# Kernel tuning notes

Measured on AMD Instinct MI355X. Metric: run time of the kernel, lower is better.

The kernel has to match this reference:

```python
import jax, jax.numpy as jnp
import numpy as np

# Performer/FAVOR+ style linear attention constants (from module __init__)
A_CONST = 0.1
S_CONST = 1.0
B_CONST = (S_CONST * (1.0 - 4.0 * A_CONST)) ** 0.5  # sqrt(0.6)
C_CONST = -(S_CONST + 1.0) / 2.0                    # -1.0

R = 256     # number of random features
D = 64      # head / feature dim
L = 65536   # sequence length
DV = 64     # value dim
SCALE = 0.125  # keep ||q||^2 ~ 1 so exp stays well-conditioned


def setup_inputs() -> dict:
    key = jax.random.key(0)
    kq, kk, kv, kw = jax.random.split(key, 4)
    Q = jax.random.normal(kq, (D, L), dtype=jnp.float32) * SCALE
    K = jax.random.normal(kk, (D, L), dtype=jnp.float32) * SCALE
    V = jax.random.normal(kv, (L, DV), dtype=jnp.float32)
    W = jax.random.normal(kw, (R, D), dtype=jnp.float32)  # random feature projections
    return {"Q": Q, "K": K, "V": V, "W": W}


def _phi(W, X, c):
    # X: [d, L]; W: [r, d] -> features [r, L]
    d = X.shape[0]
    D_norm = (1.0 - 4.0 * A_CONST) ** (d / 4.0)  # pow(pow(1-4A,0.25), d)
    sq = jnp.sum(X * X, axis=0)                  # [L], diag of X^T X
    return D_norm * jnp.exp(A_CONST + B_CONST * (W @ X) + c * sq)


def reference(Q, K, V, W):
    phiK = _phi(W, K, C_CONST * S_CONST)  # f2: [r, Lk]
    kv = phiK @ V                          # [r, dv]
    phiQ = _phi(W, Q, C_CONST)             # f1: [r, Lq]
    return phiQ.T @ kv                     # [Lq, dv]
```

## Files before the change

kernel.cpp:

```cpp
#include <hip/hip_runtime.h>

typedef _Float16 f16;
typedef __attribute__((ext_vector_type(8))) _Float16 f16x8;
typedef __attribute__((ext_vector_type(4))) _Float16 f16x4;
typedef __attribute__((ext_vector_type(4))) float f32x4;

#define BARRIER()                                              \
    do {                                                       \
        asm volatile("s_waitcnt lgkmcnt(0)" ::: "memory");     \
        __builtin_amdgcn_s_barrier();                          \
        __builtin_amdgcn_sched_barrier(0);                     \
    } while (0)

namespace {
constexpr int kL   = 65536;
constexpr int kR   = 256;
constexpr int kD   = 64;
constexpr int kDV  = 64;

constexpr int kABlocks = 512;
constexpr int kBBlocks = 512;
constexpr int kRBlocks = 128;

constexpr float kAc  = 0.1f;
constexpr float kBc  = 0.7745966692414834f;
constexpr float kDnS = 0.2888816545234944f;
constexpr float kOutScale = 9.5367431640625e-7f;
}

__global__ __launch_bounds__(512, 2)
void favor_kv(const float* __restrict__ Kg, const float* __restrict__ Vg,
              const float* __restrict__ Wg, f16* __restrict__ partials)
{
    __shared__ f16 sXt[64 * 64];
    __shared__ f16 sVt[64 * 64];
    __shared__ f16 sPhi[256 * 64];
    __shared__ float sRed[8 * 64];
    __shared__ float sRedT[64];

    const int tid  = threadIdx.x;
    const int w    = tid >> 6;
    const int lane = tid & 63;
    const int l15  = lane & 15;
    const int lhi  = lane >> 4;
    const int blk  = blockIdx.x;
    const int lblk = blk * 128;

    const int scol  = lane;
    const int dbase = w * 8;

    float ka[2][8], va[2][8];
#pragma unroll
    for (int c = 0; c < 2; ++c) {
        const int l0 = lblk + c * 64;
#pragma unroll
        for (int j = 0; j < 8; ++j) ka[c][j] = Kg[(dbase + j) * kL + l0 + scol];
#pragma unroll
        for (int j = 0; j < 8; ++j) va[c][j] = Vg[(size_t)(l0 + dbase + j) * kDV + scol];
    }

    f16x8 wfrag[2][2];
#pragma unroll
    for (int ri = 0; ri < 2; ++ri)
#pragma unroll
        for (int ks = 0; ks < 2; ++ks) {
            const float* p = Wg + (32 * w + 16 * ri + l15) * kD + 32 * ks + 8 * lhi;
            f16x8 v;
#pragma unroll
            for (int j = 0; j < 8; ++j) v[j] = (f16)p[j];
            wfrag[ri][ks] = v;
        }

    f32x4 acc[4][2];
#pragma unroll
    for (int a = 0; a < 4; ++a)
#pragma unroll
        for (int d = 0; d < 2; ++d) { f32x4 z0 = {0.f, 0.f, 0.f, 0.f}; acc[a][d] = z0; }

    const int wr = w >> 1;
    const int wc = w & 1;

#pragma unroll
    for (int c = 0; c < 2; ++c) {
        {
            float s = 0.f;
            f16x8 hk, hv;
#pragma unroll
            for (int j = 0; j < 8; ++j) {
                const float x = ka[c][j];
                s += x * x;
                hk[j] = (f16)x;
                hv[j] = (f16)va[c][j];
            }
            sRed[w * 64 + scol] = s;
            *(f16x8*)&sXt[scol * 64 + (dbase ^ ((scol & 7) << 3))] = hk;
            *(f16x8*)&sVt[scol * 64 + (dbase ^ ((scol & 7) << 3))] = hv;
        }
        BARRIER();

        {
            float sqv = 0.f;
#pragma unroll
            for (int g = 0; g < 8; ++g) sqv += sRed[g * 64 + lane];
            sRedT[lane] = sqv;
        }

#pragma unroll
        for (int ri = 0; ri < 2; ++ri) {
            f32x4 z[4];
#pragma unroll
            for (int lf = 0; lf < 4; ++lf) { f32x4 z0 = {0.f, 0.f, 0.f, 0.f}; z[lf] = z0; }
            __builtin_amdgcn_s_setprio(1);
#pragma unroll
            for (int ks = 0; ks < 2; ++ks) {
                f16x8 bfr[4];
#pragma unroll
                for (int lf = 0; lf < 4; ++lf) {
                    const int row = 16 * lf + l15;
                    bfr[lf] = *(const f16x8*)&sXt[row * 64 + ((32 * ks + 8 * lhi) ^ ((row & 7) << 3))];
                }
#pragma unroll
                for (int lf = 0; lf < 4; ++lf)
                    z[lf] = __builtin_amdgcn_mfma_f32_16x16x32_f16(bfr[lf], wfrag[ri][ks], z[lf], 0, 0, 0);
            }
            __builtin_amdgcn_s_setprio(0);
            const int r = 32 * w + 16 * ri + l15;
#pragma unroll
            for (int lf = 0; lf < 4; ++lf) {
                const f32x4 sq4 = *(const f32x4*)&sRedT[16 * lf + 4 * lhi];
                f16x4 ph;
#pragma unroll
                for (int j = 0; j < 4; ++j)
                    ph[j] = (f16)(kDnS * __expf(kAc + kBc * z[lf][j] - sq4[j]));
                const int lbase = 16 * lf + 4 * lhi;
                *(f16x4*)&sPhi[r * 64 + (lbase ^ ((r & 7) << 3))] = ph;
            }
        }
        BARRIER();

        __builtin_amdgcn_s_setprio(1);
#pragma unroll
        for (int ks = 0; ks < 2; ++ks) {
            f16x8 af[4], bf[2];
#pragma unroll
            for (int ai = 0; ai < 4; ++ai) {
                const int r = 64 * wr + 16 * ai + l15;
                af[ai] = *(const f16x8*)&sPhi[r * 64 + ((32 * ks + 8 * lhi) ^ ((r & 7) << 3))];
            }
#pragma unroll
            for (int di = 0; di < 2; ++di) {
                const int dv = 32 * wc + 16 * di + l15;
                bf[di] = *(const f16x8*)&sVt[dv * 64 + ((32 * ks + 8 * lhi) ^ ((dv & 7) << 3))];
            }
#pragma unroll
            for (int ai = 0; ai < 4; ++ai)
#pragma unroll
                for (int di = 0; di < 2; ++di)
                    acc[ai][di] = __builtin_amdgcn_mfma_f32_16x16x32_f16(af[ai], bf[di], acc[ai][di], 0, 0, 0);
        }
        __builtin_amdgcn_s_setprio(0);
        if (c == 0) BARRIER();
    }

    f16* po = partials + (size_t)blk * (kR * kDV);
#pragma unroll
    for (int ai = 0; ai < 4; ++ai)
#pragma unroll
        for (int di = 0; di < 2; ++di) {
            const int dv = 32 * wc + 16 * di + l15;
            f16x4 pk;
#pragma unroll
            for (int j = 0; j < 4; ++j) pk[j] = (f16)acc[ai][di][j];
            *(f16x4*)&po[dv * kR + 64 * wr + 16 * ai + 4 * lhi] = pk;
        }
}

__global__ __launch_bounds__(512)
void favor_reduce(const f16* __restrict__ partials, f16* __restrict__ kvT)
{
    __shared__ float sAcc[32][128];
    const int tid  = threadIdx.x;
    const int slot = tid & 15;
    const int g    = tid >> 4;
    const size_t obase = (size_t)blockIdx.x * 128 + slot * 8;

    float a[8] = {0.f, 0.f, 0.f, 0.f, 0.f, 0.f, 0.f, 0.f};
#pragma unroll 4
    for (int i = 0; i < 16; ++i) {
        const int s = g * 16 + i;
        const f16x8 v = *(const f16x8*)&partials[(size_t)s * (kR * kDV) + obase];
#pragma unroll
        for (int j = 0; j < 8; ++j) a[j] += (float)v[j];
    }
#pragma unroll
    for (int j = 0; j < 8; ++j) sAcc[g][slot * 8 + j] = a[j];
    __syncthreads();

    if (tid < 128) {
        float tot = 0.f;
#pragma unroll
        for (int gg = 0; gg < 32; ++gg) tot += sAcc[gg][tid];
        kvT[(size_t)blockIdx.x * 128 + tid] = (f16)tot;
    }
}

__global__ __launch_bounds__(512, 2)
void favor_out(const float* __restrict__ Qg, const float* __restrict__ Wg,
               const f16* __restrict__ kvT, float* __restrict__ outg)
{
    __shared__ f16 sXt[64 * 64];
    __shared__ f16 sPhiT[64 * 256];
    __shared__ f16 sKv[64 * 256];
    __shared__ float sRed[8 * 64];

    const int tid  = threadIdx.x;
    const int w    = tid >> 6;
    const int lane = tid & 63;
    const int l15  = lane & 15;
    const int lhi  = lane >> 4;
    const int blk  = blockIdx.x;
    const int lblk = blk * 128;

    const int scol  = lane;
    const int dbase = w * 8;

    float qa[2][8];
#pragma unroll
    for (int c = 0; c < 2; ++c)
#pragma unroll
        for (int j = 0; j < 8; ++j)
            qa[c][j] = Qg[(dbase + j) * kL + lblk + c * 64 + scol];

    const int kdv  = tid >> 3;
    const int kslt = tid & 7;
    f16x8 kvld[4];
#pragma unroll
    for (int m = 0; m < 4; ++m)
        kvld[m] = *(const f16x8*)&kvT[kdv * kR + kslt * 32 + 8 * m];

    f16x8 wfrag[2][2];
#pragma unroll
    for (int ri = 0; ri < 2; ++ri)
#pragma unroll
        for (int ks = 0; ks < 2; ++ks) {
            const float* p = Wg + (32 * w + 16 * ri + l15) * kD + 32 * ks + 8 * lhi;
            f16x8 v;
#pragma unroll
            for (int j = 0; j < 8; ++j) v[j] = (f16)p[j];
            wfrag[ri][ks] = v;
        }

    const int lfo = w >> 1;
    const int dvh = w & 1;

#pragma unroll
    for (int c = 0; c < 2; ++c) {
        {
            float s = 0.f;
            f16x8 hq;
#pragma unroll
            for (int j = 0; j < 8; ++j) {
                const float x = qa[c][j];
                s += x * x;
                hq[j] = (f16)x;
            }
            sRed[w * 64 + scol] = s;
            *(f16x8*)&sXt[scol * 64 + (dbase ^ ((scol & 7) << 3))] = hq;
        }
        if (c == 0) {
#pragma unroll
            for (int m = 0; m < 4; ++m)
                *(f16x8*)&sKv[kdv * kR + ((kslt * 32 + 8 * m) ^ ((kdv & 7) << 3))] = kvld[m];
        }
        BARRIER();

        float sqv = 0.f;
#pragma unroll
        for (int g = 0; g < 8; ++g) sqv += sRed[g * 64 + lane];
        float sqs[4];
#pragma unroll
        for (int lf = 0; lf < 4; ++lf) sqs[lf] = __shfl(sqv, lf * 16 + l15, 64);

#pragma unroll
        for (int ri = 0; ri < 2; ++ri) {
            f32x4 z[4];
#pragma unroll
            for (int lf = 0; lf < 4; ++lf) { f32x4 z0 = {0.f, 0.f, 0.f, 0.f}; z[lf] = z0; }
            __builtin_amdgcn_s_setprio(1);
#pragma unroll
            for (int ks = 0; ks < 2; ++ks) {
                f16x8 bfr[4];
#pragma unroll
                for (int lf = 0; lf < 4; ++lf) {
                    const int row = 16 * lf + l15;
                    bfr[lf] = *(const f16x8*)&sXt[row * 64 + ((32 * ks + 8 * lhi) ^ ((row & 7) << 3))];
                }
#pragma unroll
                for (int lf = 0; lf < 4; ++lf)
                    z[lf] = __builtin_amdgcn_mfma_f32_16x16x32_f16(wfrag[ri][ks], bfr[lf], z[lf], 0, 0, 0);
            }
            __builtin_amdgcn_s_setprio(0);
            const int r0 = 32 * w + 16 * ri + 4 * lhi;
#pragma unroll
            for (int lf = 0; lf < 4; ++lf) {
                const int lc = 16 * lf + l15;
                f16x4 ph;
#pragma unroll
                for (int j = 0; j < 4; ++j)
                    ph[j] = (f16)(kDnS * __expf(kAc + kBc * z[lf][j] - sqs[lf]));
                *(f16x4*)&sPhiT[lc * 256 + (r0 ^ ((lc & 7) << 3))] = ph;
            }
        }
        BARRIER();

        f32x4 o2[2];
        { f32x4 z0 = {0.f, 0.f, 0.f, 0.f}; o2[0] = z0; o2[1] = z0; }
        const int lrow = 16 * lfo + l15;
        __builtin_amdgcn_s_setprio(1);
#pragma unroll
        for (int ks = 0; ks < 8; ++ks) {
            const f16x8 af = *(const f16x8*)&sPhiT[lrow * 256 + ((32 * ks + 8 * lhi) ^ ((lrow & 7) << 3))];
#pragma unroll
            for (int di = 0; di < 2; ++di) {
                const int dv = 32 * dvh + 16 * di + l15;
                const f16x8 bf = *(const f16x8*)&sKv[dv * kR + ((32 * ks + 8 * lhi) ^ ((dv & 7) << 3))];
                o2[di] = __builtin_amdgcn_mfma_f32_16x16x32_f16(af, bf, o2[di], 0, 0, 0);
            }
        }
        __builtin_amdgcn_s_setprio(0);
        const int l0 = lblk + c * 64;
#pragma unroll
        for (int di = 0; di < 2; ++di)
#pragma unroll
            for (int j = 0; j < 4; ++j) {
                const int ll = 16 * lfo + 4 * lhi + j;
                const int dv = 32 * dvh + 16 * di + l15;
                outg[(size_t)(l0 + ll) * kDV + dv] = o2[di][j] * kOutScale;
            }
        if (c == 0) BARRIER();
    }
}

extern "C" void kernel_launch(void* const* d_in, const int* in_sizes, int n_in,
                              void* d_out, int out_size, void* d_ws, size_t ws_size,
                              hipStream_t stream)
{
    const float* Q = (const float*)d_in[0];
    const float* K = (const float*)d_in[1];
    const float* V = (const float*)d_in[2];
    const float* W = (const float*)d_in[3];
    float* out = (float*)d_out;

    f16* partials = (f16*)d_ws;
    f16* kvT = (f16*)((char*)d_ws + (size_t)kABlocks * kR * kDV * sizeof(f16));

    favor_kv<<<kABlocks, 512, 0, stream>>>(K, V, W, partials);
    favor_reduce<<<kRBlocks, 512, 0, stream>>>(partials, kvT);
    favor_out<<<kBBlocks, 512, 0, stream>>>(Q, W, kvT, out);

    (void)in_sizes; (void)n_in; (void)out_size; (void)ws_size;
}
```

Baseline: 41.63 us.

## Double-buffer staging, fold exp constants, keep kv fragments in registers

Both feature kernels now keep two shared-memory copies of the staged X/V tiles and row norms, so the second chunk can be staged while the first chunk's phi is computed. This cuts one barrier per kernel and lets more work overlap. The constants A and the D-norm factor are folded into a single additive base inside exp, which leaves one FMA plus exp per element. favor_out also loads the kv matrix straight into per-wave register fragments instead of staging it through shared memory, trading register pressure for less LDS traffic and smaller LDS footprint.

New measurement: 42.66 us. 2.5% more time.

```diff
diff --git a/kernel.cpp b/kernel.cpp
--- a/kernel.cpp
+++ b/kernel.cpp
@@ -22,9 +22,8 @@
 constexpr int kBBlocks = 512;
 constexpr int kRBlocks = 128;
 
-constexpr float kAc  = 0.1f;
-constexpr float kBc  = 0.7745966692414834f;
-constexpr float kDnS = 0.2888816545234944f;
+constexpr float kBc   = 0.7745966692414834f;
+constexpr float kBase0 = -1.1417405264f;
 constexpr float kOutScale = 9.5367431640625e-7f;
 }
 
@@ -32,11 +31,11 @@
 void favor_kv(const float* __restrict__ Kg, const float* __restrict__ Vg,
               const float* __restrict__ Wg, f16* __restrict__ partials)
 {
-    __shared__ f16 sXt[64 * 64];
-    __shared__ f16 sVt[64 * 64];
+    __shared__ f16 sXt[2][64 * 64];
+    __shared__ f16 sVt[2][64 * 64];
     __shared__ f16 sPhi[256 * 64];
-    __shared__ float sRed[8 * 64];
-    __shared__ float sRedT[64];
+    __shared__ float sRed[2][8 * 64];
+    __shared__ float sRedT[2][64];
 
     const int tid  = threadIdx.x;
     const int w    = tid >> 6;
@@ -80,31 +79,36 @@
     const int wr = w >> 1;
     const int wc = w & 1;
 
-#pragma unroll
-    for (int c = 0; c < 2; ++c) {
-        {
-            float s = 0.f;
-            f16x8 hk, hv;
-#pragma unroll
-            for (int j = 0; j < 8; ++j) {
-                const float x = ka[c][j];
-                s += x * x;
-                hk[j] = (f16)x;
-                hv[j] = (f16)va[c][j];
-            }
-            sRed[w * 64 + scol] = s;
-            *(f16x8*)&sXt[scol * 64 + (dbase ^ ((scol & 7) << 3))] = hk;
-            *(f16x8*)&sVt[scol * 64 + (dbase ^ ((scol & 7) << 3))] = hv;
-        }
-        BARRIER();
-
-        {
-            float sqv = 0.f;
-#pragma unroll
-            for (int g = 0; g < 8; ++g) sqv += sRed[g * 64 + lane];
-            sRedT[lane] = sqv;
-        }
-
+    auto stage = [&](int c) {
+        float s = 0.f;
+        f16x8 hk, hv;
+#pragma unroll
+        for (int j = 0; j < 8; ++j) {
+            const float x = ka[c][j];
+            s += x * x;
+            hk[j] = (f16)x;
+            hv[j] = (f16)va[c][j];
+        }
+        sRed[c][w * 64 + scol] = s;
+        *(f16x8*)&sXt[c][scol * 64 + (dbase ^ ((scol & 7) << 3))] = hk;
+        *(f16x8*)&sVt[c][scol * 64 + (dbase ^ ((scol & 7) << 3))] = hv;
+    };
+
+    auto norms = [&](int c) {
+        float sqv = 0.f;
+#pragma unroll
+        for (int g = 0; g < 8; ++g) sqv += sRed[c][g * 64 + lane];
+        sRedT[c][lane] = sqv;
+    };
+
+    auto zphi = [&](int c) {
+        f32x4 base4[4];
+#pragma unroll
+        for (int lf = 0; lf < 4; ++lf) {
+            const f32x4 sq4 = *(const f32x4*)&sRedT[c][16 * lf + 4 * lhi];
+#pragma unroll
+            for (int j = 0; j < 4; ++j) base4[lf][j] = kBase0 - sq4[j];
+        }
 #pragma unroll
         for (int ri = 0; ri < 2; ++ri) {
             f32x4 z[4];
@@ -117,7 +121,7 @@
 #pragma unroll
                 for (int lf = 0; lf < 4; ++lf) {
                     const int row = 16 * lf + l15;
-                    bfr[lf] = *(const f16x8*)&sXt[row * 64 + ((32 * ks + 8 * lhi) ^ ((row & 7) << 3))];
+                    bfr[lf] = *(const f16x8*)&sXt[c][row * 64 + ((32 * ks + 8 * lhi) ^ ((row & 7) << 3))];
                 }
 #pragma unroll
                 for (int lf = 0; lf < 4; ++lf)
@@ -127,17 +131,17 @@
             const int r = 32 * w + 16 * ri + l15;
 #pragma unroll
             for (int lf = 0; lf < 4; ++lf) {
-                const f32x4 sq4 = *(const f32x4*)&sRedT[16 * lf + 4 * lhi];
                 f16x4 ph;
 #pragma unroll
                 for (int j = 0; j < 4; ++j)
-                    ph[j] = (f16)(kDnS * __expf(kAc + kBc * z[lf][j] - sq4[j]));
+                    ph[j] = (f16)__expf(fmaf(z[lf][j], kBc, base4[lf][j]));
                 const int lbase = 16 * lf + 4 * lhi;
                 *(f16x4*)&sPhi[r * 64 + (lbase ^ ((r & 7) << 3))] = ph;
             }
         }
-        BARRIER();
-
+    };
+
+    auto pv = [&](int c) {
         __builtin_amdgcn_s_setprio(1);
 #pragma unroll
         for (int ks = 0; ks < 2; ++ks) {
@@ -150,7 +154,7 @@
 #pragma unroll
             for (int di = 0; di < 2; ++di) {
                 const int dv = 32 * wc + 16 * di + l15;
-                bf[di] = *(const f16x8*)&sVt[dv * 64 + ((32 * ks + 8 * lhi) ^ ((dv & 7) << 3))];
+                bf[di] = *(const f16x8*)&sVt[c][dv * 64 + ((32 * ks + 8 * lhi) ^ ((dv & 7) << 3))];
             }
 #pragma unroll
             for (int ai = 0; ai < 4; ++ai)
@@ -159,8 +163,20 @@
                     acc[ai][di] = __builtin_amdgcn_mfma_f32_16x16x32_f16(af[ai], bf[di], acc[ai][di], 0, 0, 0);
         }
         __builtin_amdgcn_s_setprio(0);
-        if (c == 0) BARRIER();
-    }
+    };
+
+    stage(0);
+    BARRIER();
+    norms(0);
+    zphi(0);
+    stage(1);
+    BARRIER();
+    norms(1);
+    pv(0);
+    BARRIER();
+    zphi(1);
+    BARRIER();
+    pv(1);
 
     f16* po = partials + (size_t)blk * (kR * kDV);
 #pragma unroll
@@ -208,10 +224,9 @@
 void favor_out(const float* __restrict__ Qg, const float* __restrict__ Wg,
                const f16* __restrict__ kvT, float* __restrict__ outg)
 {
-    __shared__ f16 sXt[64 * 64];
+    __shared__ f16 sXt[2][64 * 64];
     __shared__ f16 sPhiT[64 * 256];
-    __shared__ f16 sKv[64 * 256];
-    __shared__ float sRed[8 * 64];
+    __shared__ float sRed[2][8 * 64];
 
     const int tid  = threadIdx.x;
     const int w    = tid >> 6;
@@ -223,6 +238,8 @@
 
     const int scol  = lane;
     const int dbase = w * 8;
+    const int lfo = w >> 1;
+    const int dvh = w & 1;
 
     float qa[2][8];
 #pragma unroll
@@ -231,12 +248,14 @@
         for (int j = 0; j < 8; ++j)
             qa[c][j] = Qg[(dbase + j) * kL + lblk + c * 64 + scol];
 
-    const int kdv  = tid >> 3;
-    const int kslt = tid & 7;
-    f16x8 kvld[4];
-#pragma unroll
-    for (int m = 0; m < 4; ++m)
-        kvld[m] = *(const f16x8*)&kvT[kdv * kR + kslt * 32 + 8 * m];
+    f16x8 kvf[2][8];
+#pragma unroll
+    for (int di = 0; di < 2; ++di) {
+        const int dv = 32 * dvh + 16 * di + l15;
+#pragma unroll
+        for (int ks = 0; ks < 8; ++ks)
+            kvf[di][ks] = *(const f16x8*)&kvT[dv * kR + 32 * ks + 8 * lhi];
+    }
 
     f16x8 wfrag[2][2];
 #pragma unroll
@@ -250,36 +269,27 @@
             wfrag[ri][ks] = v;
         }
 
-    const int lfo = w >> 1;
-    const int dvh = w & 1;
-
-#pragma unroll
-    for (int c = 0; c < 2; ++c) {
-        {
-            float s = 0.f;
-            f16x8 hq;
-#pragma unroll
-            for (int j = 0; j < 8; ++j) {
-                const float x = qa[c][j];
-                s += x * x;
-                hq[j] = (f16)x;
-            }
-            sRed[w * 64 + scol] = s;
-            *(f16x8*)&sXt[scol * 64 + (dbase ^ ((scol & 7) << 3))] = hq;
-        }
-        if (c == 0) {
-#pragma unroll
-            for (int m = 0; m < 4; ++m)
-                *(f16x8*)&sKv[kdv * kR + ((kslt * 32 + 8 * m) ^ ((kdv & 7) << 3))] = kvld[m];
-        }
-        BARRIER();
-
+    auto stageQ = [&](int c) {
+        float s = 0.f;
+        f16x8 hq;
+#pragma unroll
+        for (int j = 0; j < 8; ++j) {
+            const float x = qa[c][j];
+            s += x * x;
+            hq[j] = (f16)x;
+        }
+        sRed[c][w * 64 + scol] = s;
+        *(f16x8*)&sXt[c][scol * 64 + (dbase ^ ((scol & 7) << 3))] = hq;
+    };
+
+    auto zphiQ = [&](int c) {
         float sqv = 0.f;
 #pragma unroll
-        for (int g = 0; g < 8; ++g) sqv += sRed[g * 64 + lane];
-        float sqs[4];
-#pragma unroll
-        for (int lf = 0; lf < 4; ++lf) sqs[lf] = __shfl(sqv, lf * 16 + l15, 64);
+        for (int g = 0; g < 8; ++g) sqv += sRed[c][g * 64 + lane];
+        float tbase[4];
+#pragma unroll
+        for (int lf = 0; lf < 4; ++lf)
+            tbase[lf] = kBase0 - __shfl(sqv, lf * 16 + l15, 64);
 
 #pragma unroll
         for (int ri = 0; ri < 2; ++ri) {
@@ -293,7 +303,7 @@
 #pragma unroll
                 for (int lf = 0; lf < 4; ++lf) {
                     const int row = 16 * lf + l15;
-                    bfr[lf] = *(const f16x8*)&sXt[row * 64 + ((32 * ks + 8 * lhi) ^ ((row & 7) << 3))];
+                    bfr[lf] = *(const f16x8*)&sXt[c][row * 64 + ((32 * ks + 8 * lhi) ^ ((row & 7) << 3))];
                 }
 #pragma unroll
                 for (int lf = 0; lf < 4; ++lf)
@@ -307,12 +317,13 @@
                 f16x4 ph;
 #pragma unroll
                 for (int j = 0; j < 4; ++j)
-                    ph[j] = (f16)(kDnS * __expf(kAc + kBc * z[lf][j] - sqs[lf]));
+                    ph[j] = (f16)__expf(fmaf(z[lf][j], kBc, tbase[lf]));
                 *(f16x4*)&sPhiT[lc * 256 + (r0 ^ ((lc & 7) << 3))] = ph;
             }
         }
-        BARRIER();
-
+    };
+
+    auto pvOut = [&](int c) {
         f32x4 o2[2];
         { f32x4 z0 = {0.f, 0.f, 0.f, 0.f}; o2[0] = z0; o2[1] = z0; }
         const int lrow = 16 * lfo + l15;
@@ -321,11 +332,8 @@
         for (int ks = 0; ks < 8; ++ks) {
             const f16x8 af = *(const f16x8*)&sPhiT[lrow * 256 + ((32 * ks + 8 * lhi) ^ ((lrow & 7) << 3))];
 #pragma unroll
-            for (int di = 0; di < 2; ++di) {
-                const int dv = 32 * dvh + 16 * di + l15;
-                const f16x8 bf = *(const f16x8*)&sKv[dv * kR + ((32 * ks + 8 * lhi) ^ ((dv & 7) << 3))];
-                o2[di] = __builtin_amdgcn_mfma_f32_16x16x32_f16(af, bf, o2[di], 0, 0, 0);
-            }
+            for (int di = 0; di < 2; ++di)
+                o2[di] = __builtin_amdgcn_mfma_f32_16x16x32_f16(af, kvf[di][ks], o2[di], 0, 0, 0);
         }
         __builtin_amdgcn_s_setprio(0);
         const int l0 = lblk + c * 64;
@@ -337,8 +345,18 @@
                 const int dv = 32 * dvh + 16 * di + l15;
                 outg[(size_t)(l0 + ll) * kDV + dv] = o2[di][j] * kOutScale;
             }
-        if (c == 0) BARRIER();
-    }
+    };
+
+    stageQ(0);
+    BARRIER();
+    zphiQ(0);
+    stageQ(1);
+    BARRIER();
+    pvOut(0);
+    BARRIER();
+    zphiQ(1);
+    BARRIER();
+    pvOut(1);
 }
 
 extern "C" void kernel_launch(void* const* d_in, const int* in_sizes, int n_in,
```

## Halve per-block sequence tile, prepack W fragments, keep kv in registers

Applied to the files above, without the earlier changes.

Both the kv and out kernels now process 64 sequence columns per block instead of two 64-column chunks, doubling the grid to 1024 blocks and removing the inner loop and its barriers. The reduce kernel sums twice as many partials and block 0 also prepacks W into f16 MFMA fragment order, so the out kernel loads W fragments directly. The out kernel holds kv fragments in registers instead of staging them through LDS. The exp argument is folded into a single fma with a combined constant. This trades more partial traffic and reduce work for higher parallelism, less LDS and less per-block setup.

New measurement: 52.80 us. 26.8% more time.

```diff
diff --git a/kernel.cpp b/kernel.cpp
--- a/kernel.cpp
+++ b/kernel.cpp
@@ -18,13 +18,12 @@
 constexpr int kD   = 64;
 constexpr int kDV  = 64;
 
-constexpr int kABlocks = 512;
-constexpr int kBBlocks = 512;
+constexpr int kABlocks = 1024;
+constexpr int kBBlocks = 1024;
 constexpr int kRBlocks = 128;
 
-constexpr float kAc  = 0.1f;
-constexpr float kBc  = 0.7745966692414834f;
-constexpr float kDnS = 0.2888816545234944f;
+constexpr float kBc   = 0.7745966692414834f;
+constexpr float kBase0 = -1.1417405264f;
 constexpr float kOutScale = 9.5367431640625e-7f;
 }
 
@@ -44,20 +43,18 @@
     const int l15  = lane & 15;
     const int lhi  = lane >> 4;
     const int blk  = blockIdx.x;
-    const int lblk = blk * 128;
+    const int l0   = blk * 64;
 
     const int scol  = lane;
     const int dbase = w * 8;
-
-    float ka[2][8], va[2][8];
-#pragma unroll
-    for (int c = 0; c < 2; ++c) {
-        const int l0 = lblk + c * 64;
-#pragma unroll
-        for (int j = 0; j < 8; ++j) ka[c][j] = Kg[(dbase + j) * kL + l0 + scol];
-#pragma unroll
-        for (int j = 0; j < 8; ++j) va[c][j] = Vg[(size_t)(l0 + dbase + j) * kDV + scol];
-    }
+    const int wr = w >> 1;
+    const int wc = w & 1;
+
+    float ka[8], va[8];
+#pragma unroll
+    for (int j = 0; j < 8; ++j) ka[j] = Kg[(dbase + j) * kL + l0 + scol];
+#pragma unroll
+    for (int j = 0; j < 8; ++j) va[j] = Vg[(size_t)(l0 + dbase + j) * kDV + scol];
 
     f16x8 wfrag[2][2];
 #pragma unroll
@@ -71,96 +68,89 @@
             wfrag[ri][ks] = v;
         }
 
+    {
+        float s = 0.f;
+        f16x8 hk, hv;
+#pragma unroll
+        for (int j = 0; j < 8; ++j) {
+            const float x = ka[j];
+            s += x * x;
+            hk[j] = (f16)x;
+            hv[j] = (f16)va[j];
+        }
+        sRed[w * 64 + scol] = s;
+        *(f16x8*)&sXt[scol * 64 + (dbase ^ ((scol & 7) << 3))] = hk;
+        *(f16x8*)&sVt[scol * 64 + (dbase ^ ((scol & 7) << 3))] = hv;
+    }
+    BARRIER();
+
+    {
+        float sqv = 0.f;
+#pragma unroll
+        for (int g = 0; g < 8; ++g) sqv += sRed[g * 64 + lane];
+        sRedT[lane] = sqv;
+    }
+
+#pragma unroll
+    for (int ri = 0; ri < 2; ++ri) {
+        f32x4 z[4];
+#pragma unroll
+        for (int lf = 0; lf < 4; ++lf) { f32x4 z0 = {0.f, 0.f, 0.f, 0.f}; z[lf] = z0; }
+        __builtin_amdgcn_s_setprio(1);
+#pragma unroll
+        for (int ks = 0; ks < 2; ++ks) {
+            f16x8 bfr[4];
+#pragma unroll
+            for (int lf = 0; lf < 4; ++lf) {
+                const int row = 16 * lf + l15;
+                bfr[lf] = *(const f16x8*)&sXt[row * 64 + ((32 * ks + 8 * lhi) ^ ((row & 7) << 3))];
+            }
+#pragma unroll
+            for (int lf = 0; lf < 4; ++lf)
+                z[lf] = __builtin_amdgcn_mfma_f32_16x16x32_f16(bfr[lf], wfrag[ri][ks], z[lf], 0, 0, 0);
+        }
+        __builtin_amdgcn_s_setprio(0);
+        const int r = 32 * w + 16 * ri + l15;
+#pragma unroll
+        for (int lf = 0; lf < 4; ++lf) {
+            const f32x4 sq4 = *(const f32x4*)&sRedT[16 * lf + 4 * lhi];
+            f16x4 ph;
+#pragma unroll
+            for (int j = 0; j < 4; ++j)
+                ph[j] = (f16)__expf(fmaf(z[lf][j], kBc, kBase0 - sq4[j]));
+            const int lbase = 16 * lf + 4 * lhi;
+            *(f16x4*)&sPhi[r * 64 + (lbase ^ ((r & 7) << 3))] = ph;
+        }
+    }
+    BARRIER();
+
     f32x4 acc[4][2];
 #pragma unroll
     for (int a = 0; a < 4; ++a)
 #pragma unroll
         for (int d = 0; d < 2; ++d) { f32x4 z0 = {0.f, 0.f, 0.f, 0.f}; acc[a][d] = z0; }
 
-    const int wr = w >> 1;
-    const int wc = w & 1;
-
-#pragma unroll
-    for (int c = 0; c < 2; ++c) {
-        {
-            float s = 0.f;
-            f16x8 hk, hv;
-#pragma unroll
-            for (int j = 0; j < 8; ++j) {
-                const float x = ka[c][j];
-                s += x * x;
-                hk[j] = (f16)x;
-                hv[j] = (f16)va[c][j];
-            }
-            sRed[w * 64 + scol] = s;
-            *(f16x8*)&sXt[scol * 64 + (dbase ^ ((scol & 7) << 3))] = hk;
-            *(f16x8*)&sVt[scol * 64 + (dbase ^ ((scol & 7) << 3))] = hv;
-        }
-        BARRIER();
-
-        {
-            float sqv = 0.f;
-#pragma unroll
-            for (int g = 0; g < 8; ++g) sqv += sRed[g * 64 + lane];
-            sRedT[lane] = sqv;
-        }
-
-#pragma unroll
-        for (int ri = 0; ri < 2; ++ri) {
-            f32x4 z[4];
-#pragma unroll
-            for (int lf = 0; lf < 4; ++lf) { f32x4 z0 = {0.f, 0.f, 0.f, 0.f}; z[lf] = z0; }
-            __builtin_amdgcn_s_setprio(1);
-#pragma unroll
-            for (int ks = 0; ks < 2; ++ks) {
-                f16x8 bfr[4];
-#pragma unroll
-                for (int lf = 0; lf < 4; ++lf) {
-                    const int row = 16 * lf + l15;
-                    bfr[lf] = *(const f16x8*)&sXt[row * 64 + ((32 * ks + 8 * lhi) ^ ((row & 7) << 3))];
-                }
-#pragma unroll
-                for (int lf = 0; lf < 4; ++lf)
-                    z[lf] = __builtin_amdgcn_mfma_f32_16x16x32_f16(bfr[lf], wfrag[ri][ks], z[lf], 0, 0, 0);
-            }
-            __builtin_amdgcn_s_setprio(0);
-            const int r = 32 * w + 16 * ri + l15;
-#pragma unroll
-            for (int lf = 0; lf < 4; ++lf) {
-                const f32x4 sq4 = *(const f32x4*)&sRedT[16 * lf + 4 * lhi];
-                f16x4 ph;
-#pragma unroll
-                for (int j = 0; j < 4; ++j)
-                    ph[j] = (f16)(kDnS * __expf(kAc + kBc * z[lf][j] - sq4[j]));
-                const int lbase = 16 * lf + 4 * lhi;
-                *(f16x4*)&sPhi[r * 64 + (lbase ^ ((r & 7) << 3))] = ph;
-            }
-        }
-        BARRIER();
-
-        __builtin_amdgcn_s_setprio(1);
-#pragma unroll
-        for (int ks = 0; ks < 2; ++ks) {
-            f16x8 af[4], bf[2];
-#pragma unroll
-            for (int ai = 0; ai < 4; ++ai) {
-                const int r = 64 * wr + 16 * ai + l15;
-                af[ai] = *(const f16x8*)&sPhi[r * 64 + ((32 * ks + 8 * lhi) ^ ((r & 7) << 3))];
-            }
-#pragma unroll
-            for (int di = 0; di < 2; ++di) {
-                const int dv = 32 * wc + 16 * di + l15;
-                bf[di] = *(const f16x8*)&sVt[dv * 64 + ((32 * ks + 8 * lhi) ^ ((dv & 7) << 3))];
-            }
-#pragma unroll
-            for (int ai = 0; ai < 4; ++ai)
-#pragma unroll
-                for (int di = 0; di < 2; ++di)
-                    acc[ai][di] = __builtin_amdgcn_mfma_f32_16x16x32_f16(af[ai], bf[di], acc[ai][di], 0, 0, 0);
-        }
-        __builtin_amdgcn_s_setprio(0);
-        if (c == 0) BARRIER();
-    }
+    __builtin_amdgcn_s_setprio(1);
+#pragma unroll
+    for (int ks = 0; ks < 2; ++ks) {
+        f16x8 af[4], bf[2];
+#pragma unroll
+        for (int ai = 0; ai < 4; ++ai) {
+            const int r = 64 * wr + 16 * ai + l15;
+            af[ai] = *(const f16x8*)&sPhi[r * 64 + ((32 * ks + 8 * lhi) ^ ((r & 7) << 3))];
+        }
+#pragma unroll
+        for (int di = 0; di < 2; ++di) {
+            const int dv = 32 * wc + 16 * di + l15;
+            bf[di] = *(const f16x8*)&sVt[dv * 64 + ((32 * ks + 8 * lhi) ^ ((dv & 7) << 3))];
+        }
+#pragma unroll
+        for (int ai = 0; ai < 4; ++ai)
+#pragma unroll
+            for (int di = 0; di < 2; ++di)
+                acc[ai][di] = __builtin_amdgcn_mfma_f32_16x16x32_f16(af[ai], bf[di], acc[ai][di], 0, 0, 0);
+    }
+    __builtin_amdgcn_s_setprio(0);
 
     f16* po = partials + (size_t)blk * (kR * kDV);
 #pragma unroll
@@ -176,18 +166,34 @@
 }
 
 __global__ __launch_bounds__(512)
-void favor_reduce(const f16* __restrict__ partials, f16* __restrict__ kvT)
+void favor_reduce(const f16* __restrict__ partials, f16* __restrict__ kvT,
+                  const float* __restrict__ Wg, f16* __restrict__ Wp)
 {
     __shared__ float sAcc[32][128];
     const int tid  = threadIdx.x;
     const int slot = tid & 15;
     const int g    = tid >> 4;
+
+    if (blockIdx.x == 0) {
+#pragma unroll
+        for (int it = 0; it < 4; ++it) {
+            const int idx    = tid + it * 512;
+            const int fragid = idx >> 6;
+            const int ln     = idx & 63;
+            const int rf = fragid >> 1, ks = fragid & 1;
+            const float* src = Wg + (16 * rf + (ln & 15)) * kD + 32 * ks + 8 * (ln >> 4);
+            f16x8 v;
+#pragma unroll
+            for (int j = 0; j < 8; ++j) v[j] = (f16)src[j];
+            *(f16x8*)&Wp[(size_t)idx * 8] = v;
+        }
+    }
+
     const size_t obase = (size_t)blockIdx.x * 128 + slot * 8;
-
     float a[8] = {0.f, 0.f, 0.f, 0.f, 0.f, 0.f, 0.f, 0.f};
-#pragma unroll 4
-    for (int i = 0; i < 16; ++i) {
-        const int s = g * 16 + i;
+#pragma unroll 8
+    for (int i = 0; i < 32; ++i) {
+        const int s = g * 32 + i;
         const f16x8 v = *(const f16x8*)&partials[(size_t)s * (kR * kDV) + obase];
 #pragma unroll
         for (int j = 0; j < 8; ++j) a[j] += (float)v[j];
@@ -205,12 +211,11 @@
 }
 
 __global__ __launch_bounds__(512, 2)
-void favor_out(const float* __restrict__ Qg, const float* __restrict__ Wg,
+void favor_out(const float* __restrict__ Qg, const f16* __restrict__ Wp,
                const f16* __restrict__ kvT, float* __restrict__ outg)
 {
     __shared__ f16 sXt[64 * 64];
     __shared__ f16 sPhiT[64 * 256];
-    __shared__ f16 sKv[64 * 256];
     __shared__ float sRed[8 * 64];
 
     const int tid  = threadIdx.x;
@@ -218,127 +223,108 @@
     const int lane = tid & 63;
     const int l15  = lane & 15;
     const int lhi  = lane >> 4;
-    const int blk  = blockIdx.x;
-    const int lblk = blk * 128;
+    const int l0   = blockIdx.x * 64;
 
     const int scol  = lane;
     const int dbase = w * 8;
-
-    float qa[2][8];
-#pragma unroll
-    for (int c = 0; c < 2; ++c)
-#pragma unroll
-        for (int j = 0; j < 8; ++j)
-            qa[c][j] = Qg[(dbase + j) * kL + lblk + c * 64 + scol];
-
-    const int kdv  = tid >> 3;
-    const int kslt = tid & 7;
-    f16x8 kvld[4];
-#pragma unroll
-    for (int m = 0; m < 4; ++m)
-        kvld[m] = *(const f16x8*)&kvT[kdv * kR + kslt * 32 + 8 * m];
-
-    f16x8 wfrag[2][2];
-#pragma unroll
-    for (int ri = 0; ri < 2; ++ri)
-#pragma unroll
-        for (int ks = 0; ks < 2; ++ks) {
-            const float* p = Wg + (32 * w + 16 * ri + l15) * kD + 32 * ks + 8 * lhi;
-            f16x8 v;
-#pragma unroll
-            for (int j = 0; j < 8; ++j) v[j] = (f16)p[j];
-            wfrag[ri][ks] = v;
-        }
-
     const int lfo = w >> 1;
     const int dvh = w & 1;
 
-#pragma unroll
-    for (int c = 0; c < 2; ++c) {
-        {
-            float s = 0.f;
-            f16x8 hq;
-#pragma unroll
-            for (int j = 0; j < 8; ++j) {
-                const float x = qa[c][j];
-                s += x * x;
-                hq[j] = (f16)x;
+    float qa[8];
+#pragma unroll
+    for (int j = 0; j < 8; ++j)
+        qa[j] = Qg[(dbase + j) * kL + l0 + scol];
+
+    f16x8 kvf[2][8];
+#pragma unroll
+    for (int di = 0; di < 2; ++di) {
+        const int dv = 32 * dvh + 16 * di + l15;
+#pragma unroll
+        for (int ks = 0; ks < 8; ++ks)
+            kvf[di][ks] = *(const f16x8*)&kvT[dv * kR + 32 * ks + 8 * lhi];
+    }
+
+    f16x8 wfrag[2][2];
+#pragma unroll
+    for (int ri = 0; ri < 2; ++ri)
+#pragma unroll
+        for (int ks = 0; ks < 2; ++ks)
+            wfrag[ri][ks] = *(const f16x8*)&Wp[(size_t)((((2 * w + ri) * 2 + ks) * 64) + lane) * 8];
+
+    {
+        float s = 0.f;
+        f16x8 hq;
+#pragma unroll
+        for (int j = 0; j < 8; ++j) {
+            const float x = qa[j];
+            s += x * x;
+            hq[j] = (f16)x;
+        }
+        sRed[w * 64 + scol] = s;
+        *(f16x8*)&sXt[scol * 64 + (dbase ^ ((scol & 7) << 3))] = hq;
+    }
+    BARRIER();
+
+    float sqv = 0.f;
+#pragma unroll
+    for (int g = 0; g < 8; ++g) sqv += sRed[g * 64 + lane];
+    float tbase[4];
+#pragma unroll
+    for (int lf = 0; lf < 4; ++lf)
+        tbase[lf] = kBase0 - __shfl(sqv, lf * 16 + l15, 64);
+
+#pragma unroll
+    for (int ri = 0; ri < 2; ++ri) {
+        f32x4 z[4];
+#pragma unroll
+        for (int lf = 0; lf < 4; ++lf) { f32x4 z0 = {0.f, 0.f, 0.f, 0.f}; z[lf] = z0; }
+        __builtin_amdgcn_s_setprio(1);
+#pragma unroll
+        for (int ks = 0; ks < 2; ++ks) {
+            f16x8 bfr[4];
+#pragma unroll
+            for (int lf = 0; lf < 4; ++lf) {
+                const int row = 16 * lf + l15;
+                bfr[lf] = *(const f16x8*)&sXt[row * 64 + ((32 * ks + 8 * lhi) ^ ((row & 7) << 3))];
             }
-            sRed[w * 64 + scol] = s;
-            *(f16x8*)&sXt[scol * 64 + (dbase ^ ((scol & 7) << 3))] = hq;
-        }
-        if (c == 0) {
-#pragma unroll
-            for (int m = 0; m < 4; ++m)
-                *(f16x8*)&sKv[kdv * kR + ((kslt * 32 + 8 * m) ^ ((kdv & 7) << 3))] = kvld[m];
-        }
-        BARRIER();
-
-        float sqv = 0.f;
-#pragma unroll
-        for (int g = 0; g < 8; ++g) sqv += sRed[g * 64 + lane];
-        float sqs[4];
-#pragma unroll
-        for (int lf = 0; lf < 4; ++lf) sqs[lf] = __shfl(sqv, lf * 16 + l15, 64);
-
-#pragma unroll
-        for (int ri = 0; ri < 2; ++ri) {
-            f32x4 z[4];
-#pragma unroll
-            for (int lf = 0; lf < 4; ++lf) { f32x4 z0 = {0.f, 0.f, 0.f, 0.f}; z[lf] = z0; }
-            __builtin_amdgcn_s_setprio(1);
-#pragma unroll
-            for (int ks = 0; ks < 2; ++ks) {
-                f16x8 bfr[4];
-#pragma unroll
-                for (int lf = 0; lf < 4; ++lf) {
-                    const int row = 16 * lf + l15;
-                    bfr[lf] = *(const f16x8*)&sXt[row * 64 + ((32 * ks + 8 * lhi) ^ ((row & 7) << 3))];
-                }
-#pragma unroll
-                for (int lf = 0; lf < 4; ++lf)
-                    z[lf] = __builtin_amdgcn_mfma_f32_16x16x32_f16(wfrag[ri][ks], bfr[lf], z[lf], 0, 0, 0);
-            }
-            __builtin_amdgcn_s_setprio(0);
-            const int r0 = 32 * w + 16 * ri + 4 * lhi;
-#pragma unroll
-            for (int lf = 0; lf < 4; ++lf) {
-                const int lc = 16 * lf + l15;
-                f16x4 ph;
-#pragma unroll
-                for (int j = 0; j < 4; ++j)
-                    ph[j] = (f16)(kDnS * __expf(kAc + kBc * z[lf][j] - sqs[lf]));
-                *(f16x4*)&sPhiT[lc * 256 + (r0 ^ ((lc & 7) << 3))] = ph;
-            }
-        }
-        BARRIER();
-
-        f32x4 o2[2];
-        { f32x4 z0 = {0.f, 0.f, 0.f, 0.f}; o2[0] = z0; o2[1] = z0; }
-        const int lrow = 16 * lfo + l15;
-        __builtin_amdgcn_s_setprio(1);
-#pragma unroll
-        for (int ks = 0; ks < 8; ++ks) {
-            const f16x8 af = *(const f16x8*)&sPhiT[lrow * 256 + ((32 * ks + 8 * lhi) ^ ((lrow & 7) << 3))];
-#pragma unroll
-            for (int di = 0; di < 2; ++di) {
-                const int dv = 32 * dvh + 16 * di + l15;
-                const f16x8 bf = *(const f16x8*)&sKv[dv * kR + ((32 * ks + 8 * lhi) ^ ((dv & 7) << 3))];
-                o2[di] = __builtin_amdgcn_mfma_f32_16x16x32_f16(af, bf, o2[di], 0, 0, 0);
-            }
+#pragma unroll
+            for (int lf = 0; lf < 4; ++lf)
+                z[lf] = __builtin_amdgcn_mfma_f32_16x16x32_f16(wfrag[ri][ks], bfr[lf], z[lf], 0, 0, 0);
         }
         __builtin_amdgcn_s_setprio(0);
-        const int l0 = lblk + c * 64;
+        const int r0 = 32 * w + 16 * ri + 4 * lhi;
+#pragma unroll
+        for (int lf = 0; lf < 4; ++lf) {
+            const int lc = 16 * lf + l15;
+            f16x4 ph;
+#pragma unroll
+            for (int j = 0; j < 4; ++j)
+                ph[j] = (f16)__expf(fmaf(z[lf][j], kBc, tbase[lf]));
+            *(f16x4*)&sPhiT[lc * 256 + (r0 ^ ((lc & 7) << 3))] = ph;
+        }
+    }
+    BARRIER();
+
+    f32x4 o2[2];
+    { f32x4 z0 = {0.f, 0.f, 0.f, 0.f}; o2[0] = z0; o2[1] = z0; }
+    const int lrow = 16 * lfo + l15;
+    __builtin_amdgcn_s_setprio(1);
+#pragma unroll
+    for (int ks = 0; ks < 8; ++ks) {
+        const f16x8 af = *(const f16x8*)&sPhiT[lrow * 256 + ((32 * ks + 8 * lhi) ^ ((lrow & 7) << 3))];
 #pragma unroll
         for (int di = 0; di < 2; ++di)
-#pragma unroll
-            for (int j = 0; j < 4; ++j) {
-                const int ll = 16 * lfo + 4 * lhi + j;
-                const int dv = 32 * dvh + 16 * di + l15;
-                outg[(size_t)(l0 + ll) * kDV + dv] = o2[di][j] * kOutScale;
-            }
-        if (c == 0) BARRIER();
-    }
+            o2[di] = __builtin_amdgcn_mfma_f32_16x16x32_f16(af, kvf[di][ks], o2[di], 0, 0, 0);
+    }
+    __builtin_amdgcn_s_setprio(0);
+#pragma unroll
+    for (int di = 0; di < 2; ++di)
+#pragma unroll
+        for (int j = 0; j < 4; ++j) {
+            const int ll = 16 * lfo + 4 * lhi + j;
+            const int dv = 32 * dvh + 16 * di + l15;
+            outg[(size_t)(l0 + ll) * kDV + dv] = o2[di][j] * kOutScale;
+        }
 }
 
 extern "C" void kernel_launch(void* const* d_in, const int* in_sizes, int n_in,
@@ -353,10 +339,11 @@
 
     f16* partials = (f16*)d_ws;
     f16* kvT = (f16*)((char*)d_ws + (size_t)kABlocks * kR * kDV * sizeof(f16));
+    f16* Wp  = kvT + (size_t)kR * kDV;
 
     favor_kv<<<kABlocks, 512, 0, stream>>>(K, V, W, partials);
-    favor_reduce<<<kRBlocks, 512, 0, stream>>>(partials, kvT);
-    favor_out<<<kBBlocks, 512, 0, stream>>>(Q, W, kvT, out);
+    favor_reduce<<<kRBlocks, 512, 0, stream>>>(partials, kvT, W, Wp);
+    favor_out<<<kBBlocks, 512, 0, stream>>>(Q, Wp, kvT, out);
 
     (void)in_sizes; (void)n_in; (void)out_size; (void)ws_size;
 }
```
